# Kernel optimization log

Hardware: AMD Instinct MI355X
Metric: run time of the kernel (lower is better)

The kernel has to match this reference:

```python
import jax, jax.numpy as jnp
import numpy as np

ALPHA = 0.2  # LeakyReLU negative slope
NEG_INF = -9e15


def setup_inputs() -> dict:
    key = jax.random.key(0)
    k_h, k_adj, k_W, k_a = jax.random.split(key, 4)
    B, N, Din, Dout = 8, 1024, 256, 256
    h = jax.random.normal(k_h, (B, N, Din), dtype=jnp.float32)
    adj = jax.random.randint(k_adj, (B, N, N), 0, 2, dtype=jnp.int32)
    # nn.Linear weight [out, in], xavier-uniform-ish init for a
    W = jax.random.normal(k_W, (Dout, Din), dtype=jnp.float32) * (1.0 / np.sqrt(Din))
    lim = np.float32(1.414 * np.sqrt(6.0 / (2 * Dout + 1)))
    a = jax.random.uniform(k_a, (2 * Dout, 1), dtype=jnp.float32, minval=-lim, maxval=lim)
    return {"h": h, "adj": adj, "W": W, "a": a}


def reference(h, adj, W, a):
    # Wh: [B, N, F]
    Wh = jnp.einsum('bnd,fd->bnf', h, W)
    F_ = Wh.shape[-1]
    # Decompose concat-then-matmul: e_ij = leakyrelu(Wh_i @ a1 + Wh_j @ a2)
    a1 = a[:F_, 0]   # [F]
    a2 = a[F_:, 0]   # [F]
    src = Wh @ a1    # [B, N]  score contribution of row node i
    dst = Wh @ a2    # [B, N]  score contribution of col node j
    e = src[:, :, None] + dst[:, None, :]          # [B, N, N]
    e = jnp.where(e > 0, e, ALPHA * e)             # LeakyReLU
    e = jnp.where(adj > 0, e, NEG_INF)             # mask non-edges
    attention = jax.nn.softmax(e, axis=-1)         # [B, N, N]
    # dropout p=0.0 -> identity in eval/train
    h_prime = jnp.einsum('bij,bjf->bif', attention, Wh)
    return h_prime
```

## Files before the change

kernel.cpp:

```cpp
#include <hip/hip_runtime.h>
#include <hip/hip_bf16.h>
#include <cstdint>

#define ALPHA 0.2f
#define NEG_INF -9000000000000000.0f

typedef __bf16 bf16_t;
typedef __bf16 bf16x8 __attribute__((ext_vector_type(8)));
typedef float f32x16 __attribute__((ext_vector_type(16)));

__global__ __launch_bounds__(256) void k_gemm1(
    const float* __restrict__ h, const float* __restrict__ W, bf16_t* __restrict__ WhT)
{
  __shared__ bf16_t WS[64 * 72];
  __shared__ bf16_t HS[64 * 72];
  const int bx = blockIdx.x;
  const int b  = bx & 7;
  const int jt = (bx >> 3) & 15;
  const int ft = bx >> 7;
  const int j0 = jt * 64, f0 = ft * 64;
  const int t = threadIdx.x;
  const int w = t >> 6, lane = t & 63;
  const int mrow = lane & 31, half = lane >> 5;
  const int fsub = (w & 1) * 32, jsub = (w >> 1) * 32;

  const int lr = t >> 2;
  const int lc = (t & 3) * 16;
  const float* wp = W + ((size_t)(f0 + lr)) * 256 + lc;
  const float* hp = h + ((size_t)(b * 1024 + j0 + lr)) * 256 + lc;

  f32x16 acc;
#pragma unroll
  for (int r = 0; r < 16; r++) acc[r] = 0.f;

  for (int s = 0; s < 4; s++) {
    if (s) __syncthreads();
    {
      float4 w0 = *(const float4*)(wp + s * 64);
      float4 w1 = *(const float4*)(wp + s * 64 + 4);
      float4 w2 = *(const float4*)(wp + s * 64 + 8);
      float4 w3 = *(const float4*)(wp + s * 64 + 12);
      bf16x8 va, vb;
      va[0] = (bf16_t)w0.x; va[1] = (bf16_t)w0.y; va[2] = (bf16_t)w0.z; va[3] = (bf16_t)w0.w;
      va[4] = (bf16_t)w1.x; va[5] = (bf16_t)w1.y; va[6] = (bf16_t)w1.z; va[7] = (bf16_t)w1.w;
      vb[0] = (bf16_t)w2.x; vb[1] = (bf16_t)w2.y; vb[2] = (bf16_t)w2.z; vb[3] = (bf16_t)w2.w;
      vb[4] = (bf16_t)w3.x; vb[5] = (bf16_t)w3.y; vb[6] = (bf16_t)w3.z; vb[7] = (bf16_t)w3.w;
      *(bf16x8*)&WS[lr * 72 + lc] = va;
      *(bf16x8*)&WS[lr * 72 + lc + 8] = vb;
      float4 h0 = *(const float4*)(hp + s * 64);
      float4 h1 = *(const float4*)(hp + s * 64 + 4);
      float4 h2 = *(const float4*)(hp + s * 64 + 8);
      float4 h3 = *(const float4*)(hp + s * 64 + 12);
      bf16x8 vc, vd;
      vc[0] = (bf16_t)h0.x; vc[1] = (bf16_t)h0.y; vc[2] = (bf16_t)h0.z; vc[3] = (bf16_t)h0.w;
      vc[4] = (bf16_t)h1.x; vc[5] = (bf16_t)h1.y; vc[6] = (bf16_t)h1.z; vc[7] = (bf16_t)h1.w;
      vd[0] = (bf16_t)h2.x; vd[1] = (bf16_t)h2.y; vd[2] = (bf16_t)h2.z; vd[3] = (bf16_t)h2.w;
      vd[4] = (bf16_t)h3.x; vd[5] = (bf16_t)h3.y; vd[6] = (bf16_t)h3.z; vd[7] = (bf16_t)h3.w;
      *(bf16x8*)&HS[lr * 72 + lc] = vc;
      *(bf16x8*)&HS[lr * 72 + lc + 8] = vd;
    }
    __syncthreads();
#pragma unroll
    for (int ks = 0; ks < 4; ks++) {
      bf16x8 af = *(const bf16x8*)&WS[(fsub + mrow) * 72 + ks * 16 + half * 8];
      bf16x8 bf = *(const bf16x8*)&HS[(jsub + mrow) * 72 + ks * 16 + half * 8];
      acc = __builtin_amdgcn_mfma_f32_32x32x16_bf16(af, bf, acc, 0, 0, 0);
    }
  }

  const int jcol = j0 + jsub + mrow;
#pragma unroll
  for (int r = 0; r < 16; r++) {
    int frow = fsub + (r & 3) + 8 * (r >> 2) + 4 * half;
    WhT[(((size_t)(b * 256 + f0 + frow)) << 10) + jcol] = (bf16_t)acc[r];
  }
}

__global__ __launch_bounds__(256) void k_src(
    const float* __restrict__ h, const float* __restrict__ W, const float* __restrict__ a,
    float* __restrict__ src, float* __restrict__ dst)
{
  __shared__ float uS[512];
  const int t = threadIdx.x;
  {
    float s1a = 0.f, s1b = 0.f, s2a = 0.f, s2b = 0.f;
#pragma unroll 4
    for (int f = 0; f < 256; f += 2) {
      float w0 = W[f * 256 + t];
      float w1 = W[(f + 1) * 256 + t];
      s1a = fmaf(w0, a[f], s1a);       s1b = fmaf(w1, a[f + 1], s1b);
      s2a = fmaf(w0, a[256 + f], s2a); s2b = fmaf(w1, a[256 + f + 1], s2b);
    }
    uS[t] = s1a + s1b; uS[256 + t] = s2a + s2b;
  }
  __syncthreads();
  const int n = t >> 4, c = t & 15;
  const int m = blockIdx.x * 16 + n;
  const float* hp = h + (size_t)m * 256 + c * 16;
  float s1 = 0.f, s2 = 0.f;
#pragma unroll
  for (int i = 0; i < 4; i++) {
    float4 v = *(const float4*)(hp + i * 4);
    const float* u1p = &uS[c * 16 + i * 4];
    const float* u2p = &uS[256 + c * 16 + i * 4];
    s1 = fmaf(v.x, u1p[0], s1); s1 = fmaf(v.y, u1p[1], s1);
    s1 = fmaf(v.z, u1p[2], s1); s1 = fmaf(v.w, u1p[3], s1);
    s2 = fmaf(v.x, u2p[0], s2); s2 = fmaf(v.y, u2p[1], s2);
    s2 = fmaf(v.z, u2p[2], s2); s2 = fmaf(v.w, u2p[3], s2);
  }
#pragma unroll
  for (int off = 8; off; off >>= 1) {
    s1 += __shfl_down(s1, off, 16);
    s2 += __shfl_down(s2, off, 16);
  }
  if (c == 0) { src[m] = s1; dst[m] = s2; }
}

__global__ __launch_bounds__(256) void k_fused(
    const bf16_t* __restrict__ WhT, const int* __restrict__ adj,
    const float* __restrict__ src, const float* __restrict__ dst,
    float* __restrict__ out)
{
  const int b  = blockIdx.x & 7;
  const int fh = (blockIdx.x >> 3) & 1;
  const int i0 = (blockIdx.x >> 4) << 5;
  const int t  = threadIdx.x;
  const int w  = t >> 6;
  const int lane = t & 63;
  const int mrow = lane & 31, half = lane >> 5;

  __shared__ float dstS[1024];
  __shared__ float srcS[32];
  __shared__ bf16_t P[2][32 * 264];

  *(float4*)&dstS[t * 4] = *(const float4*)(dst + (b << 10) + t * 4);
  if (t < 32) srcS[t] = src[(b << 10) + i0 + t];
  __syncthreads();

  f32x16 acc, acc2;
#pragma unroll
  for (int r = 0; r < 16; r++) { acc[r] = 0.f; acc2[r] = 0.f; }

  bf16x8 ones;
#pragma unroll
  for (int k = 0; k < 8; k++) ones[k] = (bf16_t)1.0f;

  const bf16_t* bp = WhT + (((size_t)(b * 256 + fh * 128 + w * 32 + mrow)) << 10);
  const int* arow = adj + ((((size_t)(b << 10)) + i0) << 10) + t;

  for (int c = 0; c < 4; c++) {
    bf16_t* Pc = &P[c & 1][0];
    {
      float dj = dstS[c * 256 + t];
      const int* ac = arow + c * 256;
#pragma unroll 8
      for (int i = 0; i < 32; i++) {
        int av = ac[(size_t)i << 10];
        float v = srcS[i] + dj;
        float vl = fmaxf(v, ALPHA * v);
        float e = (av > 0) ? vl : NEG_INF;
        Pc[i * 264 + t] = (bf16_t)__expf(e);
      }
    }
    __syncthreads();

    const bf16_t* bpc = bp + c * 256 + half * 8;
    const bf16_t* prow = Pc + mrow * 264 + half * 8;
#pragma unroll
    for (int idx = 0; idx < 16; idx++) {
      bf16x8 afr = *(const bf16x8*)(prow + idx * 16);
      bf16x8 bfr = *(const bf16x8*)(bpc + idx * 16);
      acc  = __builtin_amdgcn_mfma_f32_32x32x16_bf16(afr, bfr, acc, 0, 0, 0);
      acc2 = __builtin_amdgcn_mfma_f32_32x32x16_bf16(afr, ones, acc2, 0, 0, 0);
    }
  }

  const int col = fh * 128 + w * 32 + mrow;
#pragma unroll
  for (int r = 0; r < 16; r++) {
    int row = (r & 3) + 8 * (r >> 2) + 4 * half;
    out[((size_t)(b << 10) + i0 + row) * 256 + col] = acc[r] / acc2[r];
  }
}

extern "C" void kernel_launch(void* const* d_in, const int* in_sizes, int n_in,
                              void* d_out, int out_size, void* d_ws, size_t ws_size,
                              hipStream_t stream) {
  const float* h   = (const float*)d_in[0];
  const int*   adj = (const int*)d_in[1];
  const float* W   = (const float*)d_in[2];
  const float* a   = (const float*)d_in[3];
  float* out = (float*)d_out;

  char* wsb = (char*)d_ws;
  bf16_t* WhT = (bf16_t*)wsb;
  float* srcv = (float*)(wsb + (4u << 20));
  float* dstv = srcv + 8192;

  k_src  <<<512, 256, 0, stream>>>(h, W, a, srcv, dstv);
  k_gemm1<<<512, 256, 0, stream>>>(h, W, WhT);
  k_fused<<<512, 256, 0, stream>>>(WhT, adj, srcv, dstv, out);
}
```

Before: 139.0 us.

## Pack adjacency into bitmasks in a merged preprocessing kernel

Merges the src/dst projection kernel and the Wh GEMM kernel into one launch, and adds a step that reads the int32 adjacency once and packs it into 64-bit ballot bitmasks in workspace. The attention kernel then reads these bitmasks from shared memory instead of reading adjacency twice (once per feature half). This cuts adjacency traffic in the attention stage and removes one launch. The cost is an extra write and read of the mask buffer, plus more work placed in the preprocessing kernel.

```diff
diff --git a/kernel.cpp b/kernel.cpp
--- a/kernel.cpp
+++ b/kernel.cpp
@@ -9,117 +9,137 @@
 typedef __bf16 bf16x8 __attribute__((ext_vector_type(8)));
 typedef float f32x16 __attribute__((ext_vector_type(16)));
 
-__global__ __launch_bounds__(256) void k_gemm1(
-    const float* __restrict__ h, const float* __restrict__ W, bf16_t* __restrict__ WhT)
+__global__ __launch_bounds__(256) void k_pre(
+    const float* __restrict__ h, const float* __restrict__ W, const float* __restrict__ a,
+    const int* __restrict__ adj, bf16_t* __restrict__ WhT,
+    float* __restrict__ src, float* __restrict__ dst,
+    unsigned long long* __restrict__ mask_ws)
 {
-  __shared__ bf16_t WS[64 * 72];
-  __shared__ bf16_t HS[64 * 72];
+  __shared__ __align__(16) char smem[64 * 72 * 2 * sizeof(bf16_t)];
   const int bx = blockIdx.x;
-  const int b  = bx & 7;
-  const int jt = (bx >> 3) & 15;
-  const int ft = bx >> 7;
-  const int j0 = jt * 64, f0 = ft * 64;
   const int t = threadIdx.x;
-  const int w = t >> 6, lane = t & 63;
-  const int mrow = lane & 31, half = lane >> 5;
-  const int fsub = (w & 1) * 32, jsub = (w >> 1) * 32;
-
-  const int lr = t >> 2;
-  const int lc = (t & 3) * 16;
-  const float* wp = W + ((size_t)(f0 + lr)) * 256 + lc;
-  const float* hp = h + ((size_t)(b * 1024 + j0 + lr)) * 256 + lc;
-
-  f32x16 acc;
-#pragma unroll
-  for (int r = 0; r < 16; r++) acc[r] = 0.f;
-
-  for (int s = 0; s < 4; s++) {
-    if (s) __syncthreads();
-    {
-      float4 w0 = *(const float4*)(wp + s * 64);
-      float4 w1 = *(const float4*)(wp + s * 64 + 4);
-      float4 w2 = *(const float4*)(wp + s * 64 + 8);
-      float4 w3 = *(const float4*)(wp + s * 64 + 12);
-      bf16x8 va, vb;
-      va[0] = (bf16_t)w0.x; va[1] = (bf16_t)w0.y; va[2] = (bf16_t)w0.z; va[3] = (bf16_t)w0.w;
-      va[4] = (bf16_t)w1.x; va[5] = (bf16_t)w1.y; va[6] = (bf16_t)w1.z; va[7] = (bf16_t)w1.w;
-      vb[0] = (bf16_t)w2.x; vb[1] = (bf16_t)w2.y; vb[2] = (bf16_t)w2.z; vb[3] = (bf16_t)w2.w;
-      vb[4] = (bf16_t)w3.x; vb[5] = (bf16_t)w3.y; vb[6] = (bf16_t)w3.z; vb[7] = (bf16_t)w3.w;
-      *(bf16x8*)&WS[lr * 72 + lc] = va;
-      *(bf16x8*)&WS[lr * 72 + lc + 8] = vb;
-      float4 h0 = *(const float4*)(hp + s * 64);
-      float4 h1 = *(const float4*)(hp + s * 64 + 4);
-      float4 h2 = *(const float4*)(hp + s * 64 + 8);
-      float4 h3 = *(const float4*)(hp + s * 64 + 12);
-      bf16x8 vc, vd;
-      vc[0] = (bf16_t)h0.x; vc[1] = (bf16_t)h0.y; vc[2] = (bf16_t)h0.z; vc[3] = (bf16_t)h0.w;
-      vc[4] = (bf16_t)h1.x; vc[5] = (bf16_t)h1.y; vc[6] = (bf16_t)h1.z; vc[7] = (bf16_t)h1.w;
-      vd[0] = (bf16_t)h2.x; vd[1] = (bf16_t)h2.y; vd[2] = (bf16_t)h2.z; vd[3] = (bf16_t)h2.w;
-      vd[4] = (bf16_t)h3.x; vd[5] = (bf16_t)h3.y; vd[6] = (bf16_t)h3.z; vd[7] = (bf16_t)h3.w;
-      *(bf16x8*)&HS[lr * 72 + lc] = vc;
-      *(bf16x8*)&HS[lr * 72 + lc + 8] = vd;
+
+  if (bx < 512) {
+    bf16_t* WS = (bf16_t*)smem;
+    bf16_t* HS = WS + 64 * 72;
+    const int b  = bx & 7;
+    const int jt = (bx >> 3) & 15;
+    const int ft = bx >> 7;
+    const int j0 = jt * 64, f0 = ft * 64;
+    const int w = t >> 6, lane = t & 63;
+    const int mrow = lane & 31, half = lane >> 5;
+    const int fsub = (w & 1) * 32, jsub = (w >> 1) * 32;
+
+    const int lr = t >> 2;
+    const int lc = (t & 3) * 16;
+    const float* wp = W + ((size_t)(f0 + lr)) * 256 + lc;
+    const float* hp = h + ((size_t)(b * 1024 + j0 + lr)) * 256 + lc;
+
+    f32x16 acc;
+#pragma unroll
+    for (int r = 0; r < 16; r++) acc[r] = 0.f;
+
+    for (int s = 0; s < 4; s++) {
+      if (s) __syncthreads();
+      {
+        float4 w0 = *(const float4*)(wp + s * 64);
+        float4 w1 = *(const float4*)(wp + s * 64 + 4);
+        float4 w2 = *(const float4*)(wp + s * 64 + 8);
+        float4 w3 = *(const float4*)(wp + s * 64 + 12);
+        bf16x8 va, vb;
+        va[0] = (bf16_t)w0.x; va[1] = (bf16_t)w0.y; va[2] = (bf16_t)w0.z; va[3] = (bf16_t)w0.w;
+        va[4] = (bf16_t)w1.x; va[5] = (bf16_t)w1.y; va[6] = (bf16_t)w1.z; va[7] = (bf16_t)w1.w;
+        vb[0] = (bf16_t)w2.x; vb[1] = (bf16_t)w2.y; vb[2] = (bf16_t)w2.z; vb[3] = (bf16_t)w2.w;
+        vb[4] = (bf16_t)w3.x; vb[5] = (bf16_t)w3.y; vb[6] = (bf16_t)w3.z; vb[7] = (bf16_t)w3.w;
+        *(bf16x8*)&WS[lr * 72 + lc] = va;
+        *(bf16x8*)&WS[lr * 72 + lc + 8] = vb;
+        float4 h0 = *(const float4*)(hp + s * 64);
+        float4 h1 = *(const float4*)(hp + s * 64 + 4);
+        float4 h2 = *(const float4*)(hp + s * 64 + 8);
+        float4 h3 = *(const float4*)(hp + s * 64 + 12);
+        bf16x8 vc, vd;
+        vc[0] = (bf16_t)h0.x; vc[1] = (bf16_t)h0.y; vc[2] = (bf16_t)h0.z; vc[3] = (bf16_t)h0.w;
+        vc[4] = (bf16_t)h1.x; vc[5] = (bf16_t)h1.y; vc[6] = (bf16_t)h1.z; vc[7] = (bf16_t)h1.w;
+        vd[0] = (bf16_t)h2.x; vd[1] = (bf16_t)h2.y; vd[2] = (bf16_t)h2.z; vd[3] = (bf16_t)h2.w;
+        vd[4] = (bf16_t)h3.x; vd[5] = (bf16_t)h3.y; vd[6] = (bf16_t)h3.z; vd[7] = (bf16_t)h3.w;
+        *(bf16x8*)&HS[lr * 72 + lc] = vc;
+        *(bf16x8*)&HS[lr * 72 + lc + 8] = vd;
+      }
+      __syncthreads();
+#pragma unroll
+      for (int ks = 0; ks < 4; ks++) {
+        bf16x8 af = *(const bf16x8*)&WS[(fsub + mrow) * 72 + ks * 16 + half * 8];
+        bf16x8 bf = *(const bf16x8*)&HS[(jsub + mrow) * 72 + ks * 16 + half * 8];
+        acc = __builtin_amdgcn_mfma_f32_32x32x16_bf16(af, bf, acc, 0, 0, 0);
+      }
+    }
+
+    const int jcol = j0 + jsub + mrow;
+#pragma unroll
+    for (int r = 0; r < 16; r++) {
+      int frow = fsub + (r & 3) + 8 * (r >> 2) + 4 * half;
+      WhT[(((size_t)(b * 256 + f0 + frow)) << 10) + jcol] = (bf16_t)acc[r];
+    }
+  } else {
+    float* uS = (float*)smem;
+    const int p  = bx - 512;
+    const int m0 = p * 16;
+    {
+      float s1a = 0.f, s1b = 0.f, s2a = 0.f, s2b = 0.f;
+#pragma unroll 4
+      for (int f = 0; f < 256; f += 2) {
+        float w0 = W[f * 256 + t];
+        float w1 = W[(f + 1) * 256 + t];
+        s1a = fmaf(w0, a[f], s1a);       s1b = fmaf(w1, a[f + 1], s1b);
+        s2a = fmaf(w0, a[256 + f], s2a); s2b = fmaf(w1, a[256 + f + 1], s2b);
+      }
+      uS[t] = s1a + s1b; uS[256 + t] = s2a + s2b;
     }
     __syncthreads();
-#pragma unroll
-    for (int ks = 0; ks < 4; ks++) {
-      bf16x8 af = *(const bf16x8*)&WS[(fsub + mrow) * 72 + ks * 16 + half * 8];
-      bf16x8 bf = *(const bf16x8*)&HS[(jsub + mrow) * 72 + ks * 16 + half * 8];
-      acc = __builtin_amdgcn_mfma_f32_32x32x16_bf16(af, bf, acc, 0, 0, 0);
-    }
-  }
-
-  const int jcol = j0 + jsub + mrow;
-#pragma unroll
-  for (int r = 0; r < 16; r++) {
-    int frow = fsub + (r & 3) + 8 * (r >> 2) + 4 * half;
-    WhT[(((size_t)(b * 256 + f0 + frow)) << 10) + jcol] = (bf16_t)acc[r];
+    {
+      const int n = t >> 4, c = t & 15;
+      const int m = m0 + n;
+      const float* hp = h + (size_t)m * 256 + c * 16;
+      float s1 = 0.f, s2 = 0.f;
+#pragma unroll
+      for (int i = 0; i < 4; i++) {
+        float4 v = *(const float4*)(hp + i * 4);
+        const float* u1p = &uS[c * 16 + i * 4];
+        const float* u2p = &uS[256 + c * 16 + i * 4];
+        s1 = fmaf(v.x, u1p[0], s1); s1 = fmaf(v.y, u1p[1], s1);
+        s1 = fmaf(v.z, u1p[2], s1); s1 = fmaf(v.w, u1p[3], s1);
+        s2 = fmaf(v.x, u2p[0], s2); s2 = fmaf(v.y, u2p[1], s2);
+        s2 = fmaf(v.z, u2p[2], s2); s2 = fmaf(v.w, u2p[3], s2);
+      }
+#pragma unroll
+      for (int off = 8; off; off >>= 1) {
+        s1 += __shfl_down(s1, off, 16);
+        s2 += __shfl_down(s2, off, 16);
+      }
+      if (c == 0) { src[m] = s1; dst[m] = s2; }
+    }
+    {
+      const int wv = t >> 6, lane = t & 63;
+#pragma unroll 4
+      for (int r = 0; r < 16; r++) {
+        const size_t row = (size_t)(m0 + r);
+        const int4 av = *(const int4*)(adj + (row << 10) + 4 * t);
+        unsigned long long b0 = __ballot(av.x > 0);
+        unsigned long long b1 = __ballot(av.y > 0);
+        unsigned long long b2 = __ballot(av.z > 0);
+        unsigned long long b3 = __ballot(av.w > 0);
+        if (lane == 0) {
+          unsigned long long* mp = mask_ws + row * 16 + wv * 4;
+          mp[0] = b0; mp[1] = b1; mp[2] = b2; mp[3] = b3;
+        }
+      }
+    }
   }
 }
 
-__global__ __launch_bounds__(256) void k_src(
-    const float* __restrict__ h, const float* __restrict__ W, const float* __restrict__ a,
-    float* __restrict__ src, float* __restrict__ dst)
-{
-  __shared__ float uS[512];
-  const int t = threadIdx.x;
-  {
-    float s1a = 0.f, s1b = 0.f, s2a = 0.f, s2b = 0.f;
-#pragma unroll 4
-    for (int f = 0; f < 256; f += 2) {
-      float w0 = W[f * 256 + t];
-      float w1 = W[(f + 1) * 256 + t];
-      s1a = fmaf(w0, a[f], s1a);       s1b = fmaf(w1, a[f + 1], s1b);
-      s2a = fmaf(w0, a[256 + f], s2a); s2b = fmaf(w1, a[256 + f + 1], s2b);
-    }
-    uS[t] = s1a + s1b; uS[256 + t] = s2a + s2b;
-  }
-  __syncthreads();
-  const int n = t >> 4, c = t & 15;
-  const int m = blockIdx.x * 16 + n;
-  const float* hp = h + (size_t)m * 256 + c * 16;
-  float s1 = 0.f, s2 = 0.f;
-#pragma unroll
-  for (int i = 0; i < 4; i++) {
-    float4 v = *(const float4*)(hp + i * 4);
-    const float* u1p = &uS[c * 16 + i * 4];
-    const float* u2p = &uS[256 + c * 16 + i * 4];
-    s1 = fmaf(v.x, u1p[0], s1); s1 = fmaf(v.y, u1p[1], s1);
-    s1 = fmaf(v.z, u1p[2], s1); s1 = fmaf(v.w, u1p[3], s1);
-    s2 = fmaf(v.x, u2p[0], s2); s2 = fmaf(v.y, u2p[1], s2);
-    s2 = fmaf(v.z, u2p[2], s2); s2 = fmaf(v.w, u2p[3], s2);
-  }
-#pragma unroll
-  for (int off = 8; off; off >>= 1) {
-    s1 += __shfl_down(s1, off, 16);
-    s2 += __shfl_down(s2, off, 16);
-  }
-  if (c == 0) { src[m] = s1; dst[m] = s2; }
-}
-
-__global__ __launch_bounds__(256) void k_fused(
-    const bf16_t* __restrict__ WhT, const int* __restrict__ adj,
-    const float* __restrict__ src, const float* __restrict__ dst,
-    float* __restrict__ out)
+__global__ __launch_bounds__(256) void k_attn(
+    const bf16_t* __restrict__ WhT, const float* __restrict__ src, const float* __restrict__ dst,
+    const unsigned long long* __restrict__ mask_ws, float* __restrict__ out)
 {
   const int b  = blockIdx.x & 7;
   const int fh = (blockIdx.x >> 3) & 1;
@@ -131,10 +151,16 @@
 
   __shared__ float dstS[1024];
   __shared__ float srcS[32];
+  __shared__ unsigned long long maskS[32 * 16];
   __shared__ bf16_t P[2][32 * 264];
 
   *(float4*)&dstS[t * 4] = *(const float4*)(dst + (b << 10) + t * 4);
   if (t < 32) srcS[t] = src[(b << 10) + i0 + t];
+  {
+    const size_t mb = ((size_t)(b << 10) + i0) * 16;
+    maskS[t]       = mask_ws[mb + t];
+    maskS[t + 256] = mask_ws[mb + t + 256];
+  }
   __syncthreads();
 
   f32x16 acc, acc2;
@@ -146,19 +172,19 @@
   for (int k = 0; k < 8; k++) ones[k] = (bf16_t)1.0f;
 
   const bf16_t* bp = WhT + (((size_t)(b * 256 + fh * 128 + w * 32 + mrow)) << 10);
-  const int* arow = adj + ((((size_t)(b << 10)) + i0) << 10) + t;
 
   for (int c = 0; c < 4; c++) {
     bf16_t* Pc = &P[c & 1][0];
     {
       float dj = dstS[c * 256 + t];
-      const int* ac = arow + c * 256;
+      int mi = c * 4 + (t & 3);
+      int sh = t >> 2;
 #pragma unroll 8
       for (int i = 0; i < 32; i++) {
-        int av = ac[(size_t)i << 10];
+        unsigned long long w64 = maskS[i * 16 + mi];
         float v = srcS[i] + dj;
         float vl = fmaxf(v, ALPHA * v);
-        float e = (av > 0) ? vl : NEG_INF;
+        float e = ((w64 >> sh) & 1ull) ? vl : NEG_INF;
         Pc[i * 264 + t] = (bf16_t)__expf(e);
       }
     }
@@ -196,8 +222,8 @@
   bf16_t* WhT = (bf16_t*)wsb;
   float* srcv = (float*)(wsb + (4u << 20));
   float* dstv = srcv + 8192;
-
-  k_src  <<<512, 256, 0, stream>>>(h, W, a, srcv, dstv);
-  k_gemm1<<<512, 256, 0, stream>>>(h, W, WhT);
-  k_fused<<<512, 256, 0, stream>>>(WhT, adj, srcv, dstv, out);
+  unsigned long long* mask_ws = (unsigned long long*)(wsb + (4u << 20) + 65536);
+
+  k_pre <<<1024, 256, 0, stream>>>(h, W, a, adj, WhT, srcv, dstv, mask_ws);
+  k_attn<<<512,  256, 0, stream>>>(WhT, srcv, dstv, mask_ws, out);
 }
```

New measurement: 122.9 us. -11.6%, faster.
